# Optimization experiments

Hardware: AMD Instinct MI355X
Metric: run time of the kernel (lower is better)

The kernel has to match this reference:

```python
import jax, jax.numpy as jnp
import numpy as np

H_HEADS = 4

def setup_inputs() -> dict:
    key = jax.random.key(0)
    ks = jax.random.split(key, 14)
    B, C, H, W = 8, 512, 32, 32
    r = C // H_HEADS  # SE reduction = h per SelfModule(channel, h)
    s_in = 0.02
    inp = {
        'x': jax.random.normal(ks[0], (B, C, H, W), jnp.float32),
        'wq': jax.random.normal(ks[1], (C, C), jnp.float32) * s_in,
        'bq': jnp.zeros((C,), jnp.float32),
        'wk': jax.random.normal(ks[2], (C, C), jnp.float32) * s_in,
        'bk': jnp.zeros((C,), jnp.float32),
        'wv': jax.random.normal(ks[3], (C, C), jnp.float32) * s_in,
        'bv': jnp.zeros((C,), jnp.float32),
        'fc1_w': jax.random.normal(ks[4], (r, C), jnp.float32) * s_in,
        'fc1_b': jnp.zeros((r,), jnp.float32),
        'fc2_w': jax.random.normal(ks[5], (C, r), jnp.float32) * s_in,
        'fc2_b': jnp.zeros((C,), jnp.float32),
        'gate_w': jax.random.normal(ks[6], (1, C), jnp.float32) * s_in,
        'gate_b': jnp.zeros((1,), jnp.float32),
    }
    return inp

def _conv1x1(y, w, b):
    # y: [B,C,H,W], w: [O,C] (1x1 conv kernel squeezed), b: [O]
    return jnp.einsum('bchw,oc->bohw', y, w) + b[None, :, None, None]

def reference(x, wq, bq, wk, bk, wv, bv, fc1_w, fc1_b, fc2_w, fc2_b, gate_w, gate_b):
    B, C, H, W = x.shape
    h = H_HEADS
    dk = C // h
    N = H * W

    # --- SelfScaling (SE without final sigmoid-in-block; sigmoid applied at mul) ---
    p = x.mean(axis=(2, 3))                                   # [B,C] global avg pool
    f = jax.nn.relu(p @ fc1_w.T + fc1_b) @ fc2_w.T + fc2_b    # [B,C]
    x = x * jax.nn.sigmoid(f)[:, :, None, None] + x

    # --- RTrans: conv1x1 QKV, attention over flattened H*W ---
    q = _conv1x1(x, wq, bq).reshape(B, h, dk, N).transpose(0, 1, 3, 2)  # [B,h,N,dk]
    k = _conv1x1(x, wk, bk).reshape(B, h, dk, N)                        # [B,h,dk,N]
    v = _conv1x1(x, wv, bv).reshape(B, h, dk, N)                        # [B,h,dk,N]
    scale = 1.0 / float(np.sqrt(dk))
    att = jax.nn.softmax(jnp.einsum('bhnd,bhdm->bhnm', q, k) * scale, axis=-1)  # [B,h,N,N]
    o = jnp.einsum('bhdn,bhnm->bhdm', v, att).reshape(B, C, H, W)  # v @ att as in torch

    # --- SelfGating ---
    gate = jax.nn.sigmoid(_conv1x1(o, gate_w, gate_b))  # [B,1,H,W]
    return o * gate + o
```

## Files before the change

### kernel.cpp

```cpp
#include <hip/hip_runtime.h>
#include <hip/hip_bf16.h>

#define B_ 8
#define C_ 512
#define N_ 1024
#define HEADS_ 4
#define DK_ 128
#define R_ 128

typedef float f32x4 __attribute__((ext_vector_type(4)));
typedef __bf16 bf16x8 __attribute__((ext_vector_type(8)));
typedef unsigned short u16;

constexpr float kScale = 0.08838834764831845f;

#define OFF_P   0u
#define OFF_SS  16384u
#define OFF_WB  32768u
#define OFF_XT  1605632u
#define OFF_QT  9994240u
#define OFF_KT  18382848u
#define OFF_V   26771456u
#define OFF_DEN 35160064u
#define OFF_G   35291136u

__device__ __forceinline__ u16 f2b(float f) {
  __hip_bfloat16 h = __float2bfloat16(f);
  return __builtin_bit_cast(u16, h);
}

typedef const __attribute__((address_space(1))) unsigned int* gptr_t;
typedef __attribute__((address_space(3))) unsigned int* lptr_t;
__device__ __forceinline__ void gload16(const void* g, void* l) {
  __builtin_amdgcn_global_load_lds((gptr_t)g, (lptr_t)l, 16, 0, 0);
}

__device__ __forceinline__ f32x4 mfma16(bf16x8 a, bf16x8 b, f32x4 c) {
  return __builtin_amdgcn_mfma_f32_16x16x32_bf16(a, b, c, 0, 0, 0);
}

__global__ __launch_bounds__(64) void k_pool(const float* __restrict__ x,
                                             float* __restrict__ p) {
  int bc = blockIdx.x, lane = threadIdx.x;
  const float4* row = (const float4*)(x + (size_t)bc * N_);
  float s = 0.f;
  for (int i = lane; i < N_ / 4; i += 64) {
    float4 t = row[i];
    s += t.x + t.y + t.z + t.w;
  }
  for (int o = 32; o > 0; o >>= 1) s += __shfl_down(s, o, 64);
  if (lane == 0) p[bc] = s * (1.0f / N_);
}

__global__ __launch_bounds__(256) void k_se(const float* __restrict__ p,
                                            const float* __restrict__ fc1w,
                                            const float* __restrict__ fc1b,
                                            const float* __restrict__ fc2w,
                                            const float* __restrict__ fc2b,
                                            float* __restrict__ ss) {
  __shared__ float pl[C_];
  __shared__ float f1[R_];
  int b = blockIdx.x, t = threadIdx.x;
  for (int c = t; c < C_; c += 256) pl[c] = p[b * C_ + c];
  __syncthreads();
  if (t < R_) {
    float a = fc1b[t];
    for (int c = 0; c < C_; c++) a += pl[c] * fc1w[t * C_ + c];
    f1[t] = fmaxf(a, 0.f);
  }
  __syncthreads();
  for (int c = t; c < C_; c += 256) {
    float a = fc2b[c];
    for (int j = 0; j < R_; j++) a += f1[j] * fc2w[c * R_ + j];
    ss[b * C_ + c] = 1.f + 1.f / (1.f + __expf(-a));
  }
}

__global__ __launch_bounds__(256) void k_castw(const float* __restrict__ wq,
                                               const float* __restrict__ wk,
                                               const float* __restrict__ wv,
                                               u16* __restrict__ wb) {
  int i = blockIdx.x * 256 + threadIdx.x;
  int idx = i * 4;
  const float* srcs[3] = {wq, wk, wv};
  int w = idx / (C_ * C_), off = idx % (C_ * C_);
  float4 v = *(const float4*)(srcs[w] + off);
  u16* d = wb + idx;
  d[0] = f2b(v.x); d[1] = f2b(v.y); d[2] = f2b(v.z); d[3] = f2b(v.w);
}

__global__ __launch_bounds__(256) void k_xt(const float* __restrict__ x,
                                            const float* __restrict__ ss,
                                            u16* __restrict__ xt) {
  int b = blockIdx.z, c0 = blockIdx.y * 64, n0 = blockIdx.x * 64;
  __shared__ float tile[64][65];
  int t = threadIdx.x;
  int cr = t >> 4, nc4 = (t & 15) * 4;
  for (int j = 0; j < 4; j++) {
    int c = cr + j * 16;
    float sc = ss[b * C_ + c0 + c];
    float4 v = *(const float4*)(x + ((size_t)b * C_ + c0 + c) * N_ + n0 + nc4);
    tile[c][nc4 + 0] = v.x * sc;
    tile[c][nc4 + 1] = v.y * sc;
    tile[c][nc4 + 2] = v.z * sc;
    tile[c][nc4 + 3] = v.w * sc;
  }
  __syncthreads();
  int nr = t >> 2, cc = (t & 3) * 16;
  u16 ov[16];
  for (int m = 0; m < 16; m++) ov[m] = f2b(tile[cc + m][nr]);
  u16* dst = xt + ((size_t)b * N_ + n0 + nr) * C_ + c0 + cc;
  for (int m = 0; m < 16; m++) dst[m] = ov[m];
}

__global__ __launch_bounds__(256) void k_qkv(const u16* __restrict__ xt,
                                             const u16* __restrict__ wb,
                                             const float* __restrict__ bq,
                                             const float* __restrict__ bk,
                                             const float* __restrict__ bv,
                                             u16* __restrict__ qt,
                                             u16* __restrict__ kt,
                                             u16* __restrict__ v) {
  __shared__ char smem[32768];
  int b = blockIdx.y / 3, sel = blockIdx.y % 3;
  int tile = blockIdx.x;
  const char *Ab, *Bb;
  u16* out;
  const float* bias;
  int mt, nt, rstride;
  size_t xtoff = (size_t)b * N_ * C_;
  if (sel < 2) {
    mt = tile & 7; nt = tile >> 3;
    Ab = (const char*)(xt + xtoff + (size_t)mt * 128 * C_);
    Bb = (const char*)(wb + (size_t)sel * C_ * C_ + (size_t)nt * 128 * C_);
    out = (sel ? kt : qt) + xtoff;
    bias = sel ? bk : bq;
    rstride = C_ * 2;
  } else {
    mt = tile & 3; nt = tile >> 2;
    Ab = (const char*)(wb + (size_t)2 * C_ * C_ + (size_t)mt * 128 * C_);
    Bb = (const char*)(xt + xtoff + (size_t)nt * 128 * C_);
    out = v + (size_t)b * C_ * N_;
    bias = bv;
    rstride = N_ * 2;
  }
  int t = threadIdx.x, lane = t & 63, wid = t >> 6;
  int wr = wid >> 1, wc = wid & 1;
  const f32x4 z4 = {0.f, 0.f, 0.f, 0.f};
  f32x4 acc[4][4];
  for (int i = 0; i < 4; i++)
    for (int j = 0; j < 4; j++) acc[i][j] = z4;

  char* lA = smem;
  char* lB = smem + 16384;
  for (int ko = 0; ko < C_; ko += 64) {
    __syncthreads();
    for (int i = wid; i < 16; i += 4) {
      int beta = i * 1024 + lane * 16;
      int row = beta >> 7, cb = (beta & 127) ^ ((row & 7) << 4);
      gload16(Ab + (size_t)row * 1024 + ko * 2 + cb, lA + beta);
    }
    for (int i = wid; i < 16; i += 4) {
      int beta = i * 1024 + lane * 16;
      int row = beta >> 7, cb = (beta & 127) ^ ((row & 7) << 4);
      gload16(Bb + (size_t)row * 1024 + ko * 2 + cb, lB + beta);
    }
    __syncthreads();
    for (int ks = 0; ks < 2; ks++) {
      int kb = ks * 64 + (lane >> 4) * 16;
      bf16x8 af[4], bfr[4];
      for (int fi = 0; fi < 4; fi++) {
        int row = wr * 64 + fi * 16 + (lane & 15);
        af[fi] = *(const bf16x8*)(lA + row * 128 + (kb ^ ((row & 7) << 4)));
      }
      for (int fj = 0; fj < 4; fj++) {
        int row = wc * 64 + fj * 16 + (lane & 15);
        bfr[fj] = *(const bf16x8*)(lB + row * 128 + (kb ^ ((row & 7) << 4)));
      }
      for (int fi = 0; fi < 4; fi++)
        for (int fj = 0; fj < 4; fj++)
          acc[fi][fj] = mfma16(af[fi], bfr[fj], acc[fi][fj]);
    }
  }
  __syncthreads();
  for (int fi = 0; fi < 4; fi++)
    for (int fj = 0; fj < 4; fj++) {
      int colb = wc * 64 + fj * 16 + (lane & 15);
      for (int r = 0; r < 4; r++) {
        int rowb = wr * 64 + fi * 16 + (lane >> 4) * 4 + r;
        float bva = (sel < 2) ? bias[nt * 128 + colb] : bias[mt * 128 + rowb];
        float val = acc[fi][fj][r] + bva;
        int byte = rowb * 256 + ((colb * 2) ^ ((rowb & 7) << 4));
        *(u16*)(smem + byte) = f2b(val);
      }
    }
  __syncthreads();
  for (int i = t; i < 2048; i += 256) {
    int row = i >> 4, cb = (i & 15) * 16;
    bf16x8 val = *(const bf16x8*)(smem + row * 256 + (cb ^ ((row & 7) << 4)));
    *(bf16x8*)((char*)out + (size_t)(mt * 128 + row) * rstride + nt * 256 + cb) = val;
  }
}

__global__ __launch_bounds__(512) void k_passA(const u16* __restrict__ qt,
                                               const u16* __restrict__ kt,
                                               float* __restrict__ invden) {
  __shared__ char lK[2][32768];
  int bh = blockIdx.x, nb = blockIdx.y * 128;
  int b = bh >> 2, h = bh & 3;
  const char* qb = (const char*)(qt + (size_t)b * N_ * C_ + h * DK_);
  const char* kb = (const char*)(kt + (size_t)b * N_ * C_ + h * DK_);
  int t = threadIdx.x, lane = t & 63, wid = t >> 6;
  bf16x8 aq[4];
  {
    const char* qr = qb + (size_t)(nb + wid * 16 + (lane & 15)) * (C_ * 2);
    for (int ks = 0; ks < 4; ks++)
      aq[ks] = *(const bf16x8*)(qr + ks * 64 + (lane >> 4) * 16);
  }
  float sacc[4] = {0.f, 0.f, 0.f, 0.f};
  const f32x4 z4 = {0.f, 0.f, 0.f, 0.f};
  for (int i = wid; i < 32; i += 8) {
    int beta = i * 1024 + lane * 16;
    int row = beta >> 8, cb = (beta & 255) ^ ((row & 7) << 4);
    gload16(kb + (size_t)row * (C_ * 2) + cb, lK[0] + beta);
  }
  for (int mc = 0; mc < 8; mc++) {
    int cur = mc & 1;
    __syncthreads();
    if (mc < 7) {
      int mnext = (mc + 1) * 128;
      for (int i = wid; i < 32; i += 8) {
        int beta = i * 1024 + lane * 16;
        int row = beta >> 8, cb = (beta & 255) ^ ((row & 7) << 4);
        gload16(kb + (size_t)(mnext + row) * (C_ * 2) + cb, lK[cur ^ 1] + beta);
      }
    }
    for (int fj = 0; fj < 8; fj++) {
      f32x4 s = z4;
      for (int ks = 0; ks < 4; ks++) {
        int row = fj * 16 + (lane & 15);
        bf16x8 bk_ = *(const bf16x8*)(lK[cur] + row * 256 +
                                      ((ks * 64 + (lane >> 4) * 16) ^ ((row & 7) << 4)));
        s = mfma16(aq[ks], bk_, s);
      }
      for (int r = 0; r < 4; r++) sacc[r] += __expf(s[r] * kScale);
    }
  }
  for (int r = 0; r < 4; r++) {
    float vv = sacc[r];
    for (int m = 1; m < 16; m <<= 1) vv += __shfl_xor(vv, m, 64);
    sacc[r] = vv;
  }
  if ((lane & 15) == 0) {
    int n = nb + wid * 16 + (lane >> 4) * 4;
    for (int r = 0; r < 4; r++) invden[(size_t)bh * N_ + n + r] = 1.f / sacc[r];
  }
}

__global__ __launch_bounds__(512) void k_passB(const u16* __restrict__ qt,
                                               const u16* __restrict__ kt,
                                               const u16* __restrict__ v,
                                               const float* __restrict__ invden,
                                               const float* __restrict__ gw,
                                               float* __restrict__ out,
                                               float* __restrict__ g) {
  __shared__ char lQ[2][16384];
  __shared__ char lV[2][16384];
  __shared__ char lP[16384];
  __shared__ float gacc[128];
  int bh = blockIdx.x, mb = blockIdx.y * 128;
  int b = bh >> 2, h = bh & 3;
  const char* qb = (const char*)(qt + (size_t)b * N_ * C_ + h * DK_);
  const char* kb = (const char*)(kt + (size_t)b * N_ * C_ + h * DK_);
  const char* vb = (const char*)(v + ((size_t)b * C_ + h * DK_) * N_);
  float* ob = out + ((size_t)b * C_ + h * DK_) * N_ + mb;
  int t = threadIdx.x, lane = t & 63, wid = t >> 6;
  bf16x8 ak[4];
  {
    const char* kr = kb + (size_t)(mb + wid * 16 + (lane & 15)) * (C_ * 2);
    for (int ks = 0; ks < 4; ks++)
      ak[ks] = *(const bf16x8*)(kr + ks * 64 + (lane >> 4) * 16);
  }
  if (t < 128) gacc[t] = 0.f;
  const f32x4 z4 = {0.f, 0.f, 0.f, 0.f};
  f32x4 oacc[8];
  for (int j = 0; j < 8; j++) oacc[j] = z4;

  for (int i = wid; i < 16; i += 8) {
    int beta = i * 1024 + lane * 16;
    int row = beta >> 8, cb = (beta & 255) ^ ((row & 7) << 4);
    gload16(qb + (size_t)row * (C_ * 2) + cb, lQ[0] + beta);
  }
  for (int i = wid; i < 16; i += 8) {
    int beta = i * 1024 + lane * 16;
    int row = beta >> 7, cb = (beta & 127) ^ ((row & 7) << 4);
    gload16(vb + (size_t)row * (N_ * 2) + cb, lV[0] + beta);
  }

  for (int nc = 0; nc < 16; nc++) {
    int n0 = nc * 64, cur = nc & 1;
    __syncthreads();
    if (nc < 15) {
      int nn = n0 + 64;
      for (int i = wid; i < 16; i += 8) {
        int beta = i * 1024 + lane * 16;
        int row = beta >> 8, cb = (beta & 255) ^ ((row & 7) << 4);
        gload16(qb + (size_t)(nn + row) * (C_ * 2) + cb, lQ[cur ^ 1] + beta);
      }
      for (int i = wid; i < 16; i += 8) {
        int beta = i * 1024 + lane * 16;
        int row = beta >> 7, cb = (beta & 127) ^ ((row & 7) << 4);
        gload16(vb + (size_t)row * (N_ * 2) + nn * 2 + cb, lV[cur ^ 1] + beta);
      }
    }
    for (int fj = 0; fj < 4; fj++) {
      f32x4 s = z4;
      for (int ks = 0; ks < 4; ks++) {
        int row = fj * 16 + (lane & 15);
        bf16x8 bq_ = *(const bf16x8*)(lQ[cur] + row * 256 +
                                      ((ks * 64 + (lane >> 4) * 16) ^ ((row & 7) << 4)));
        s = mfma16(ak[ks], bq_, s);
      }
      float iden = invden[(size_t)bh * N_ + n0 + fj * 16 + (lane & 15)];
      int nl2 = (fj * 16 + (lane & 15)) * 2;
      for (int r = 0; r < 4; r++) {
        float pval = __expf(s[r] * kScale) * iden;
        int ml = wid * 16 + (lane >> 4) * 4 + r;
        *(u16*)(lP + ml * 128 + (nl2 ^ ((ml & 7) << 4))) = f2b(pval);
      }
    }
    asm volatile("s_waitcnt lgkmcnt(0)" ::: "memory");
    __builtin_amdgcn_sched_barrier(0);
    __builtin_amdgcn_s_barrier();
    for (int ks2 = 0; ks2 < 2; ks2++) {
      int kb2 = ks2 * 64 + (lane >> 4) * 16;
      int vrow = wid * 16 + (lane & 15);
      bf16x8 av = *(const bf16x8*)(lV[cur] + vrow * 128 + (kb2 ^ ((vrow & 7) << 4)));
      for (int fm = 0; fm < 8; fm++) {
        int row = fm * 16 + (lane & 15);
        bf16x8 bp = *(const bf16x8*)(lP + row * 128 + (kb2 ^ ((row & 7) << 4)));
        oacc[fm] = mfma16(av, bp, oacc[fm]);
      }
    }
  }
  float gwl[4];
  for (int r = 0; r < 4; r++)
    gwl[r] = gw[h * DK_ + wid * 16 + (lane >> 4) * 4 + r];
  __syncthreads();
  for (int fm = 0; fm < 8; fm++) {
    int m = fm * 16 + (lane & 15);
    int d = wid * 16 + (lane >> 4) * 4;
    float part = 0.f;
    for (int r = 0; r < 4; r++) {
      float val = oacc[fm][r];
      ob[(size_t)(d + r) * N_ + m] = val;
      part += gwl[r] * val;
    }
    atomicAdd(&gacc[m], part);
  }
  __syncthreads();
  if (t < 128) atomicAdd(&g[(size_t)b * N_ + mb + t], gacc[t]);
}

__global__ __launch_bounds__(256) void k_zero_g(float* __restrict__ g) {
  g[blockIdx.x * 256 + threadIdx.x] = 0.f;
}

__global__ __launch_bounds__(256) void k_gate_apply(const float* __restrict__ g,
                                                    const float* __restrict__ gb,
                                                    float* __restrict__ out) {
  size_t i = ((size_t)blockIdx.x * 256 + threadIdx.x) * 4;
  int b = (int)(i / ((size_t)C_ * N_));
  int n = (int)(i & (N_ - 1));
  float4 gv = *(const float4*)(g + (size_t)b * N_ + n);
  float bias = gb[0];
  float4 v = *(float4*)(out + i);
  v.x *= 1.f + 1.f / (1.f + __expf(-(gv.x + bias)));
  v.y *= 1.f + 1.f / (1.f + __expf(-(gv.y + bias)));
  v.z *= 1.f + 1.f / (1.f + __expf(-(gv.z + bias)));
  v.w *= 1.f + 1.f / (1.f + __expf(-(gv.w + bias)));
  *(float4*)(out + i) = v;
}

extern "C" void kernel_launch(void* const* d_in, const int* in_sizes, int n_in,
                              void* d_out, int out_size, void* d_ws, size_t ws_size,
                              hipStream_t stream) {
  const float* x    = (const float*)d_in[0];
  const float* wq   = (const float*)d_in[1];
  const float* bq   = (const float*)d_in[2];
  const float* wk   = (const float*)d_in[3];
  const float* bk   = (const float*)d_in[4];
  const float* wv   = (const float*)d_in[5];
  const float* bv   = (const float*)d_in[6];
  const float* fc1w = (const float*)d_in[7];
  const float* fc1b = (const float*)d_in[8];
  const float* fc2w = (const float*)d_in[9];
  const float* fc2b = (const float*)d_in[10];
  const float* gw   = (const float*)d_in[11];
  const float* gb   = (const float*)d_in[12];
  float* out = (float*)d_out;
  char* ws = (char*)d_ws;

  float* p   = (float*)(ws + OFF_P);
  float* ssc = (float*)(ws + OFF_SS);
  u16* wb  = (u16*)(ws + OFF_WB);
  u16* xt  = (u16*)(ws + OFF_XT);
  u16* qt  = (u16*)(ws + OFF_QT);
  u16* kt  = (u16*)(ws + OFF_KT);
  u16* v   = (u16*)(ws + OFF_V);
  float* den = (float*)(ws + OFF_DEN);
  float* g   = (float*)(ws + OFF_G);

  k_pool<<<B_ * C_, 64, 0, stream>>>(x, p);
  k_castw<<<768, 256, 0, stream>>>(wq, wk, wv, wb);
  k_se<<<B_, 256, 0, stream>>>(p, fc1w, fc1b, fc2w, fc2b, ssc);
  k_zero_g<<<B_ * N_ / 256, 256, 0, stream>>>(g);
  k_xt<<<dim3(16, 8, B_), 256, 0, stream>>>(x, ssc, xt);
  k_qkv<<<dim3(32, B_ * 3), 256, 0, stream>>>(xt, wb, bq, bk, bv, qt, kt, v);
  k_passA<<<dim3(32, 8), 512, 0, stream>>>(qt, kt, den);
  k_passB<<<dim3(32, 8), 512, 0, stream>>>(qt, kt, v, den, gw, out, g);
  k_gate_apply<<<B_ * C_ * N_ / 1024, 256, 0, stream>>>(g, gb, out);
}
```

Before: 124.7 us.

## Keep attention probabilities in registers and feed PV MFMA directly

The QK^T MFMA operands are swapped so each wave's score fragment lands in the layout a 16x16x16 bf16 MFMA needs as its B operand. P then stays in registers instead of being written to LDS and read back, which drops the lP buffer and a barrier per chunk. The PV product now uses the K=16 MFMA instruction (or a zero-padded K=32 fallback), with each wave owning 16 query columns across all 128 dk rows. This raises the number of MFMA issues and V reads from LDS, and changes the gate reduction to a single atomic per thread.

```diff
diff --git a/kernel.cpp b/kernel.cpp
--- a/kernel.cpp
+++ b/kernel.cpp
@@ -10,6 +10,7 @@
 
 typedef float f32x4 __attribute__((ext_vector_type(4)));
 typedef __bf16 bf16x8 __attribute__((ext_vector_type(8)));
+typedef short short4v __attribute__((ext_vector_type(4)));
 typedef unsigned short u16;
 
 constexpr float kScale = 0.08838834764831845f;
@@ -38,6 +39,21 @@
 __device__ __forceinline__ f32x4 mfma16(bf16x8 a, bf16x8 b, f32x4 c) {
   return __builtin_amdgcn_mfma_f32_16x16x32_bf16(a, b, c, 0, 0, 0);
 }
+
+#if __has_builtin(__builtin_amdgcn_mfma_f32_16x16x16bf16_1k)
+__device__ __forceinline__ f32x4 mfma_k16(short4v a, short4v b, f32x4 c) {
+  return __builtin_amdgcn_mfma_f32_16x16x16bf16_1k(a, b, c, 0, 0, 0);
+}
+#else
+__device__ __forceinline__ f32x4 mfma_k16(short4v a, short4v b, f32x4 c) {
+  bf16x8 a8 = {}, b8 = {};
+  for (int e = 0; e < 4; e++) {
+    ((u16*)&a8)[e] = ((u16*)&a)[e];
+    ((u16*)&b8)[e] = ((u16*)&b)[e];
+  }
+  return __builtin_amdgcn_mfma_f32_16x16x32_bf16(a8, b8, c, 0, 0, 0);
+}
+#endif
 
 __global__ __launch_bounds__(64) void k_pool(const float* __restrict__ x,
                                              float* __restrict__ p) {
@@ -266,7 +282,6 @@
                                                float* __restrict__ g) {
   __shared__ char lQ[2][16384];
   __shared__ char lV[2][16384];
-  __shared__ char lP[16384];
   __shared__ float gacc[128];
   int bh = blockIdx.x, mb = blockIdx.y * 128;
   int b = bh >> 2, h = bh & 3;
@@ -274,12 +289,13 @@
   const char* kb = (const char*)(kt + (size_t)b * N_ * C_ + h * DK_);
   const char* vb = (const char*)(v + ((size_t)b * C_ + h * DK_) * N_);
   float* ob = out + ((size_t)b * C_ + h * DK_) * N_ + mb;
+  const float* idenb = invden + (size_t)bh * N_;
   int t = threadIdx.x, lane = t & 63, wid = t >> 6;
-  bf16x8 ak[4];
+  bf16x8 bkm[4];
   {
     const char* kr = kb + (size_t)(mb + wid * 16 + (lane & 15)) * (C_ * 2);
     for (int ks = 0; ks < 4; ks++)
-      ak[ks] = *(const bf16x8*)(kr + ks * 64 + (lane >> 4) * 16);
+      bkm[ks] = *(const bf16x8*)(kr + ks * 64 + (lane >> 4) * 16);
   }
   if (t < 128) gacc[t] = 0.f;
   const f32x4 z4 = {0.f, 0.f, 0.f, 0.f};
@@ -313,51 +329,47 @@
         gload16(vb + (size_t)row * (N_ * 2) + nn * 2 + cb, lV[cur ^ 1] + beta);
       }
     }
+    short4v pf[4];
     for (int fj = 0; fj < 4; fj++) {
       f32x4 s = z4;
       for (int ks = 0; ks < 4; ks++) {
         int row = fj * 16 + (lane & 15);
-        bf16x8 bq_ = *(const bf16x8*)(lQ[cur] + row * 256 +
-                                      ((ks * 64 + (lane >> 4) * 16) ^ ((row & 7) << 4)));
-        s = mfma16(ak[ks], bq_, s);
-      }
-      float iden = invden[(size_t)bh * N_ + n0 + fj * 16 + (lane & 15)];
-      int nl2 = (fj * 16 + (lane & 15)) * 2;
-      for (int r = 0; r < 4; r++) {
-        float pval = __expf(s[r] * kScale) * iden;
-        int ml = wid * 16 + (lane >> 4) * 4 + r;
-        *(u16*)(lP + ml * 128 + (nl2 ^ ((ml & 7) << 4))) = f2b(pval);
-      }
-    }
-    asm volatile("s_waitcnt lgkmcnt(0)" ::: "memory");
-    __builtin_amdgcn_sched_barrier(0);
-    __builtin_amdgcn_s_barrier();
-    for (int ks2 = 0; ks2 < 2; ks2++) {
-      int kb2 = ks2 * 64 + (lane >> 4) * 16;
-      int vrow = wid * 16 + (lane & 15);
-      bf16x8 av = *(const bf16x8*)(lV[cur] + vrow * 128 + (kb2 ^ ((vrow & 7) << 4)));
-      for (int fm = 0; fm < 8; fm++) {
-        int row = fm * 16 + (lane & 15);
-        bf16x8 bp = *(const bf16x8*)(lP + row * 128 + (kb2 ^ ((row & 7) << 4)));
-        oacc[fm] = mfma16(av, bp, oacc[fm]);
-      }
-    }
-  }
-  float gwl[4];
-  for (int r = 0; r < 4; r++)
-    gwl[r] = gw[h * DK_ + wid * 16 + (lane >> 4) * 4 + r];
-  __syncthreads();
-  for (int fm = 0; fm < 8; fm++) {
-    int m = fm * 16 + (lane & 15);
-    int d = wid * 16 + (lane >> 4) * 4;
-    float part = 0.f;
+        bf16x8 aq = *(const bf16x8*)(lQ[cur] + row * 256 +
+                                     ((ks * 64 + (lane >> 4) * 16) ^ ((row & 7) << 4)));
+        s = mfma16(aq, bkm[ks], s);
+      }
+      float4 id4 = *(const float4*)(idenb + n0 + fj * 16 + (lane >> 4) * 4);
+      short4v pp;
+      pp[0] = (short)f2b(__expf(s[0] * kScale) * id4.x);
+      pp[1] = (short)f2b(__expf(s[1] * kScale) * id4.y);
+      pp[2] = (short)f2b(__expf(s[2] * kScale) * id4.z);
+      pp[3] = (short)f2b(__expf(s[3] * kScale) * id4.w);
+      pf[fj] = pp;
+    }
+    for (int fd = 0; fd < 8; fd++) {
+      int row = fd * 16 + (lane & 15);
+      const char* vr = lV[cur] + row * 128;
+      int sw = (row & 7) << 4;
+      for (int fj = 0; fj < 4; fj++) {
+        short4v av = *(const short4v*)(vr + ((fj * 32 + (lane >> 4) * 8) ^ sw));
+        oacc[fd] = mfma_k16(av, pf[fj], oacc[fd]);
+      }
+    }
+  }
+  __syncthreads();
+  float part = 0.f;
+  int mcol = wid * 16 + (lane & 15);
+  for (int fd = 0; fd < 8; fd++) {
+    float4 gwv = *(const float4*)(gw + h * DK_ + fd * 16 + (lane >> 4) * 4);
+    float gwa[4] = {gwv.x, gwv.y, gwv.z, gwv.w};
     for (int r = 0; r < 4; r++) {
-      float val = oacc[fm][r];
-      ob[(size_t)(d + r) * N_ + m] = val;
-      part += gwl[r] * val;
-    }
-    atomicAdd(&gacc[m], part);
-  }
+      float val = oacc[fd][r];
+      int d = fd * 16 + (lane >> 4) * 4 + r;
+      ob[(size_t)d * N_ + mcol] = val;
+      part += gwa[r] * val;
+    }
+  }
+  atomicAdd(&gacc[mcol], part);
   __syncthreads();
   if (t < 128) atomicAdd(&g[(size_t)b * N_ + mb + t], gacc[t]);
 }
```

Result: no change. 125.0 us (+0.2%).
